# Performance work log

Measured on AMD Instinct MI355X. Metric: run time of the kernel, lower is better.

## Reference

```python
import jax, jax.numpy as jnp
import numpy as np

B, T, D = 2, 2048, 1024
H = 16
HD = D // H            # 64 head_dim
DL = 512               # d_latent
NR = 64                # n_rope
EPS = 1.1920929e-07    # torch.finfo(float32).eps (nn.RMSNorm default)


def _rms_norm(x, w):
    # x: (..., HD); RMSNorm: x / sqrt(mean(x^2)+eps) * w
    ms = jnp.mean(jnp.square(x), axis=-1, keepdims=True)
    return x * jax.lax.rsqrt(ms + EPS) * w


def setup_inputs() -> dict:
    key = jax.random.key(0)
    ks = jax.random.split(key, 10)
    s = 0.02
    return {
        "x": jax.random.normal(ks[0], (B, T, D), dtype=jnp.float32),
        "W_DQ": jax.random.normal(ks[1], (DL, HD), dtype=jnp.float32) * s,
        "W_UQ": jax.random.normal(ks[2], (HD, DL), dtype=jnp.float32) * s,
        "W_DKV": jax.random.normal(ks[3], (2 * DL, HD), dtype=jnp.float32) * s,
        "W_UKV": jax.random.normal(ks[4], (2 * HD, 2 * DL), dtype=jnp.float32) * s,
        "W_QR": jax.random.normal(ks[5], (NR, HD), dtype=jnp.float32) * s,
        "W_KR": jax.random.normal(ks[6], (NR, HD), dtype=jnp.float32) * s,
        "W_O": jax.random.normal(ks[7], (HD, HD), dtype=jnp.float32) * s,
        "q_norm_w": jnp.ones((HD,), dtype=jnp.float32),
        "k_norm_w": jnp.ones((HD,), dtype=jnp.float32),
    }


def reference(x, W_DQ, W_UQ, W_DKV, W_UKV, W_QR, W_KR, W_O, q_norm_w, k_norm_w):
    b, t, d = x.shape
    scale = HD ** (-0.5)
    # (B, H, T, HD)
    xh = x.reshape(b, t, H, HD).transpose(0, 2, 1, 3)
    # latent down/up projections (Linear: y = x @ W.T)
    c_q = jnp.einsum('bhtd,ld->bhtl', xh, W_DQ)              # (B,H,T,DL)
    q_c = jnp.einsum('bhtl,dl->bhtd', c_q, W_UQ)             # (B,H,T,HD)
    q_c_norm = _rms_norm(q_c, q_norm_w)
    q_r = jnp.einsum('bhtd,rd->bhtr', q_c_norm, W_QR)        # rope = identity
    q = jnp.concatenate([q_c_norm, q_r], axis=-1)            # (B,H,T,HD+NR)

    c_kv = jnp.einsum('bhtd,ld->bhtl', xh, W_DKV)            # (B,H,T,2DL)
    kv = jnp.einsum('bhtl,dl->bhtd', c_kv, W_UKV)            # (B,H,T,2HD)
    k_c, v_c = kv[..., :HD], kv[..., HD:]
    k_c_norm = _rms_norm(k_c, k_norm_w)
    k_r = jnp.einsum('bhtd,rd->bhtr', xh, W_KR)              # rope = identity
    k = jnp.concatenate([k_c_norm, k_r], axis=-1)            # (B,H,T,HD+NR)

    scores = jnp.einsum('bhqd,bhkd->bhqk', q, k) * scale     # (B,H,T,T)
    causal = jnp.triu(jnp.full((t, t), -jnp.inf, dtype=scores.dtype), k=1)
    attn = jax.nn.softmax(scores + causal, axis=-1)
    ctx = jnp.einsum('bhqk,bhkd->bhqd', attn, v_c)           # (B,H,T,HD)
    out = jnp.einsum('bhtd,od->bhto', ctx, W_O)
    return out.transpose(0, 2, 1, 3).reshape(b, t, d)
```

## Files before the change

kernel.cpp:

```cpp
#include <hip/hip_runtime.h>
#include <hip/hip_bf16.h>
#include <math.h>

namespace {

constexpr int T  = 2048;
constexpr int HD = 64;
constexpr float EPS = 1.1920929e-07f;
constexpr float PS = 0.125f * 1.44269504f;

constexpr int OFF_DQ  = 0;
constexpr int OFF_UQ  = 32768;
constexpr int OFF_DKV = 65536;
constexpr int OFF_UKV = 131072;
constexpr int OFF_QR  = 262144;
constexpr int OFF_KR  = 266240;
constexpr int OFF_O   = 270336;
constexpr int W_TOTAL = 274432;

typedef __attribute__((ext_vector_type(8))) short bf8v;
typedef __attribute__((ext_vector_type(4))) float f4v;

#define MFMA16(a, b, c) __builtin_amdgcn_mfma_f32_16x16x32_bf16((a), (b), (c), 0, 0, 0)

__device__ __forceinline__ short f2bf(float f) {
  union { float f; unsigned u; } v; v.f = f;
  unsigned r = v.u + 0x7FFFu + ((v.u >> 16) & 1u);
  return (short)(r >> 16);
}

__device__ __forceinline__ f4v z4() { f4v z = {0.f, 0.f, 0.f, 0.f}; return z; }

__device__ __forceinline__ int swz128(int b) { return b ^ (((b >> 7) & 7) << 4); }
__device__ __forceinline__ int swz256(int b) { return b ^ (((b >> 8) & 7) << 4); }

__device__ __forceinline__ bf8v ldA128(const short* lds, int row, int k) {
  return *(const bf8v*)((const char*)lds + swz128(row * 128 + k * 2));
}
__device__ __forceinline__ bf8v ldA256(const short* lds, int row, int k) {
  return *(const bf8v*)((const char*)lds + swz256(row * 256 + k * 2));
}

__device__ __forceinline__ void stage64x64(short* lds, const short* src, int stride, int tid) {
#pragma unroll
  for (int p = 0; p < 2; ++p) {
    int ci = tid + p * 256;
    int r = ci >> 3, c = (ci & 7) << 3;
    bf8v v = *(const bf8v*)(src + (size_t)r * stride + c);
    *(bf8v*)((char*)lds + swz128(ci * 16)) = v;
  }
}
__device__ __forceinline__ void stage128x64(short* lds, const short* src, int stride, int tid) {
#pragma unroll
  for (int p = 0; p < 4; ++p) {
    int ci = tid + p * 256;
    int r = ci >> 3, c = (ci & 7) << 3;
    bf8v v = *(const bf8v*)(src + (size_t)r * stride + c);
    *(bf8v*)((char*)lds + swz128(ci * 16)) = v;
  }
}

__device__ __forceinline__ void scat128(short* lds, int row0, int lane, int nt, f4v v) {
  int col = nt * 16 + (lane & 15);
  int r0 = row0 + ((lane >> 4) << 2);
#pragma unroll
  for (int r = 0; r < 4; ++r)
    *(short*)((char*)lds + swz128((r0 + r) * 128 + col * 2)) = f2bf(v[r]);
}
__device__ __forceinline__ void scat256(short* lds, int row0, int lane, int col, f4v v) {
  int r0 = row0 + ((lane >> 4) << 2);
#pragma unroll
  for (int r = 0; r < 4; ++r)
    *(short*)((char*)lds + swz256((r0 + r) * 256 + col * 2)) = f2bf(v[r]);
}

__device__ __forceinline__ void gload_lds16(const void* g, void* l) {
  __builtin_amdgcn_global_load_lds(
      (const __attribute__((address_space(1))) void*)g,
      (__attribute__((address_space(3))) void*)l, 16, 0, 0);
}

__global__ __launch_bounds__(256) void cvt_x_kernel(const float* __restrict__ x,
                                                    short* __restrict__ xb) {
  int i = (blockIdx.x * 256 + threadIdx.x) * 4;
  float4 v = *(const float4*)(x + i);
  int d = i & 1023, t = (i >> 10) & 2047, b = i >> 21;
  int h = d >> 6, dd = d & 63;
  short4 o;
  o.x = f2bf(v.x); o.y = f2bf(v.y); o.z = f2bf(v.z); o.w = f2bf(v.w);
  *(short4*)(xb + ((((size_t)b * 16 + h) * T + t) * 64 + dd)) = o;
}

__global__ __launch_bounds__(256) void cvt_w_kernel(
    const float* __restrict__ W_DQ, const float* __restrict__ W_UQ,
    const float* __restrict__ W_DKV, const float* __restrict__ W_UKV,
    const float* __restrict__ W_QR, const float* __restrict__ W_KR,
    const float* __restrict__ W_O, short* __restrict__ wb) {
  int i = blockIdx.x * 256 + threadIdx.x;
  const float* src; int off;
  if      (i < 32768)  { src = W_DQ;  off = 0; }
  else if (i < 65536)  { src = W_UQ;  off = 32768; }
  else if (i < 131072) { src = W_DKV; off = 65536; }
  else if (i < 262144) { src = W_UKV; off = 131072; }
  else if (i < 266240) { src = W_QR;  off = 262144; }
  else if (i < 270336) { src = W_KR;  off = 266240; }
  else                 { src = W_O;   off = 270336; }
  wb[i] = f2bf(src[i - off]);
}

__global__ __launch_bounds__(256) void proj_q_mfma(
    const short* __restrict__ xb, const short* __restrict__ wb,
    const float* __restrict__ qnw, short* __restrict__ qb) {
  __shared__ __attribute__((aligned(16))) short Xs[64 * 64];
  __shared__ __attribute__((aligned(16))) short Wd[64 * 64];
  __shared__ __attribute__((aligned(16))) short Wu[64 * 64];
  __shared__ __attribute__((aligned(16))) short Cs[64 * 64];
  __shared__ __attribute__((aligned(16))) short Qr[64 * 64];

  const int tid = threadIdx.x, lane = tid & 63, w = tid >> 6;
  const int bh = blockIdx.y, t0 = blockIdx.x * 64;
  const int arow = w * 16 + (lane & 15);
  const int koff = (lane >> 4) << 3;

  stage64x64(Xs, xb + ((size_t)bh * T + t0) * 64, 64, tid);

  f4v acc[4];
#pragma unroll
  for (int nt = 0; nt < 4; ++nt) acc[nt] = z4();

  for (int lc = 0; lc < 8; ++lc) {
    const int l0 = lc * 64;
    __syncthreads();
    stage64x64(Wd, wb + OFF_DQ + (size_t)l0 * 64, 64, tid);
    stage64x64(Wu, wb + OFF_UQ + l0, 512, tid);
    __syncthreads();
    f4v cc[4];
#pragma unroll
    for (int nt = 0; nt < 4; ++nt) cc[nt] = z4();
#pragma unroll
    for (int ks = 0; ks < 2; ++ks) {
      bf8v a = ldA128(Xs, arow, ks * 32 + koff);
#pragma unroll
      for (int nt = 0; nt < 4; ++nt) {
        bf8v b = ldA128(Wd, nt * 16 + (lane & 15), ks * 32 + koff);
        cc[nt] = MFMA16(a, b, cc[nt]);
      }
    }
#pragma unroll
    for (int nt = 0; nt < 4; ++nt) scat128(Cs, w * 16, lane, nt, cc[nt]);
#pragma unroll
    for (int ks = 0; ks < 2; ++ks) {
      bf8v a = ldA128(Cs, arow, ks * 32 + koff);
#pragma unroll
      for (int nt = 0; nt < 4; ++nt) {
        bf8v b = ldA128(Wu, nt * 16 + (lane & 15), ks * 32 + koff);
        acc[nt] = MFMA16(a, b, acc[nt]);
      }
    }
  }

  float w4[4];
#pragma unroll
  for (int nt = 0; nt < 4; ++nt) w4[nt] = qnw[nt * 16 + (lane & 15)] * PS;
  f4v qn[4];
#pragma unroll
  for (int r = 0; r < 4; ++r) {
    float ss = 0.f;
#pragma unroll
    for (int nt = 0; nt < 4; ++nt) ss += acc[nt][r] * acc[nt][r];
    ss += __shfl_xor(ss, 1, 16); ss += __shfl_xor(ss, 2, 16);
    ss += __shfl_xor(ss, 4, 16); ss += __shfl_xor(ss, 8, 16);
    float inv = rsqrtf(ss * (1.f / 64.f) + EPS);
#pragma unroll
    for (int nt = 0; nt < 4; ++nt) qn[nt][r] = acc[nt][r] * inv * w4[nt];
  }

  __syncthreads();
#pragma unroll
  for (int nt = 0; nt < 4; ++nt) scat128(Cs, w * 16, lane, nt, qn[nt]);
  stage64x64(Wd, wb + OFF_QR, 64, tid);
  __syncthreads();

  f4v qr[4];
#pragma unroll
  for (int nt = 0; nt < 4; ++nt) qr[nt] = z4();
#pragma unroll
  for (int ks = 0; ks < 2; ++ks) {
    bf8v a = ldA128(Cs, arow, ks * 32 + koff);
#pragma unroll
    for (int nt = 0; nt < 4; ++nt) {
      bf8v b = ldA128(Wd, nt * 16 + (lane & 15), ks * 32 + koff);
      qr[nt] = MFMA16(a, b, qr[nt]);
    }
  }
#pragma unroll
  for (int nt = 0; nt < 4; ++nt) scat128(Qr, w * 16, lane, nt, qr[nt]);
  __syncthreads();

  short* qdst = qb + ((size_t)bh * T + t0) * 128;
#pragma unroll
  for (int p = 0; p < 2; ++p) {
    int ci = tid + p * 256;
    int r = ci >> 3, c = (ci & 7) << 3;
    *(bf8v*)(qdst + (size_t)r * 128 + c) =
        *(const bf8v*)((const char*)Cs + swz128(ci * 16));
    *(bf8v*)(qdst + (size_t)r * 128 + 64 + c) =
        *(const bf8v*)((const char*)Qr + swz128(ci * 16));
  }
}

__global__ __launch_bounds__(256) void proj_kv_mfma(
    const short* __restrict__ xb, const short* __restrict__ wb,
    const float* __restrict__ knw, short* __restrict__ kb, short* __restrict__ vtg) {
  __shared__ __attribute__((aligned(16))) short Xs[64 * 64];
  __shared__ __attribute__((aligned(16))) short Wd[64 * 64];
  __shared__ __attribute__((aligned(16))) short Cs[64 * 64];
  __shared__ __attribute__((aligned(16))) short Wu[128 * 64];
  __shared__ __attribute__((aligned(16))) short Ko[64 * 128];
  __shared__ __attribute__((aligned(16))) short Vt[64 * 64];

  const int tid = threadIdx.x, lane = tid & 63, w = tid >> 6;
  const int bh = blockIdx.y, t0 = blockIdx.x * 64;
  const int arow = w * 16 + (lane & 15);
  const int koff = (lane >> 4) << 3;

  stage64x64(Xs, xb + ((size_t)bh * T + t0) * 64, 64, tid);

  f4v acc[8];
#pragma unroll
  for (int nt = 0; nt < 8; ++nt) acc[nt] = z4();

  for (int lc = 0; lc < 16; ++lc) {
    const int l0 = lc * 64;
    __syncthreads();
    stage64x64(Wd, wb + OFF_DKV + (size_t)l0 * 64, 64, tid);
    stage128x64(Wu, wb + OFF_UKV + l0, 1024, tid);
    __syncthreads();
    f4v cc[4];
#pragma unroll
    for (int nt = 0; nt < 4; ++nt) cc[nt] = z4();
#pragma unroll
    for (int ks = 0; ks < 2; ++ks) {
      bf8v a = ldA128(Xs, arow, ks * 32 + koff);
#pragma unroll
      for (int nt = 0; nt < 4; ++nt) {
        bf8v b = ldA128(Wd, nt * 16 + (lane & 15), ks * 32 + koff);
        cc[nt] = MFMA16(a, b, cc[nt]);
      }
    }
#pragma unroll
    for (int nt = 0; nt < 4; ++nt) scat128(Cs, w * 16, lane, nt, cc[nt]);
#pragma unroll
    for (int ks = 0; ks < 2; ++ks) {
      bf8v a = ldA128(Cs, arow, ks * 32 + koff);
#pragma unroll
      for (int nt = 0; nt < 8; ++nt) {
        bf8v b = ldA128(Wu, nt * 16 + (lane & 15), ks * 32 + koff);
        acc[nt] = MFMA16(a, b, acc[nt]);
      }
    }
  }

  float w4[4];
#pragma unroll
  for (int nt = 0; nt < 4; ++nt) w4[nt] = knw[nt * 16 + (lane & 15)];
#pragma unroll
  for (int r = 0; r < 4; ++r) {
    float ss = 0.f;
#pragma unroll
    for (int nt = 0; nt < 4; ++nt) ss += acc[nt][r] * acc[nt][r];
    ss += __shfl_xor(ss, 1, 16); ss += __shfl_xor(ss, 2, 16);
    ss += __shfl_xor(ss, 4, 16); ss += __shfl_xor(ss, 8, 16);
    float inv = rsqrtf(ss * (1.f / 64.f) + EPS);
#pragma unroll
    for (int nt = 0; nt < 4; ++nt) acc[nt][r] *= inv * w4[nt];
  }
#pragma unroll
  for (int nt = 0; nt < 4; ++nt) scat256(Ko, w * 16, lane, nt * 16 + (lane & 15), acc[nt]);
#pragma unroll
  for (int nt = 0; nt < 4; ++nt) {
    int d = nt * 16 + (lane & 15);
    int tl0 = w * 16 + ((lane >> 4) << 2);
#pragma unroll
    for (int r = 0; r < 4; ++r)
      *(short*)((char*)Vt + swz128(d * 128 + (tl0 + r) * 2)) = f2bf(acc[4 + nt][r]);
  }

  __syncthreads();
  stage64x64(Wd, wb + OFF_KR, 64, tid);
  __syncthreads();
  f4v kr[4];
#pragma unroll
  for (int nt = 0; nt < 4; ++nt) kr[nt] = z4();
#pragma unroll
  for (int ks = 0; ks < 2; ++ks) {
    bf8v a = ldA128(Xs, arow, ks * 32 + koff);
#pragma unroll
    for (int nt = 0; nt < 4; ++nt) {
      bf8v b = ldA128(Wd, nt * 16 + (lane & 15), ks * 32 + koff);
      kr[nt] = MFMA16(a, b, kr[nt]);
    }
  }
#pragma unroll
  for (int nt = 0; nt < 4; ++nt) scat256(Ko, w * 16, lane, 64 + nt * 16 + (lane & 15), kr[nt]);
  __syncthreads();

  short* kdst = kb + ((size_t)bh * T + t0) * 128;
#pragma unroll
  for (int p = 0; p < 4; ++p) {
    int ci = tid + p * 256;
    int r = ci >> 4, c = (ci & 15) << 3;
    *(bf8v*)(kdst + (size_t)r * 128 + c) =
        *(const bf8v*)((const char*)Ko + swz256(ci * 16));
  }
#pragma unroll
  for (int p = 0; p < 2; ++p) {
    int ci = tid + p * 256;
    int d = ci >> 3, c = (ci & 7) << 3;
    *(bf8v*)(vtg + ((size_t)bh * 64 + d) * T + t0 + c) =
        *(const bf8v*)((const char*)Vt + swz128(ci * 16));
  }
}

__global__ __launch_bounds__(256) void attn_mfma(
    const short* __restrict__ qb, const short* __restrict__ kb,
    const short* __restrict__ vtg, const short* __restrict__ wb,
    float* __restrict__ out) {
  __shared__ __attribute__((aligned(16))) short Ks[3][64 * 128];
  __shared__ __attribute__((aligned(16))) short Vs[2][64 * 64];
  __shared__ __attribute__((aligned(16))) short Ps[64 * 64];

  const int tid = threadIdx.x, lane = tid & 63, w = tid >> 6;
  const int lin = blockIdx.y * 16 + blockIdx.x;
  const int xcd = lin & 7, slot = lin >> 3;
  const int bh = xcd + 8 * (slot >> 4);
  const int px = slot & 15;
  const int qtA = px, qtB = 31 - px;
  const int cntA = qtA + 1;
  const int NT = 33;

  const int b = bh >> 4, h = bh & 15;
  const int c16 = lane & 15;
  const int g4 = lane >> 4;
  const int koff = g4 << 3;
  const int rg4 = g4 << 2;
  const int lbase = lane & 48;

  const short* kbh = kb + (size_t)bh * T * 128;
  const short* vbh = vtg + (size_t)bh * 64 * T;

  bf8v aqA[4], aqB[4], bwo[2][4];
  {
    const short* qA = qb + ((size_t)bh * T + qtA * 64 + w * 16 + c16) * 128;
    const short* qB = qb + ((size_t)bh * T + qtB * 64 + w * 16 + c16) * 128;
#pragma unroll
    for (int ks = 0; ks < 4; ++ks) {
      aqA[ks] = *(const bf8v*)(qA + ks * 32 + koff);
      aqB[ks] = *(const bf8v*)(qB + ks * 32 + koff);
    }
#pragma unroll
    for (int ks = 0; ks < 2; ++ks)
#pragma unroll
      for (int nt = 0; nt < 4; ++nt)
        bwo[ks][nt] = *(const bf8v*)(wb + OFF_O + (size_t)(nt * 16 + c16) * 64 +
                                     ks * 32 + koff);
  }

  auto ktile = [&](int gg) { return (gg < NT) ? ((gg < cntA) ? gg : gg - cntA) : 0; };

  auto stageK = [&](int gg) {
    const int jt = ktile(gg);
    const char* src = (const char*)(kbh + jt * 64 * 128);
    char* dst = (char*)&Ks[gg % 3][0];
#pragma unroll
    for (int p = 0; p < 4; ++p) {
      const int base = p * 256 + w * 64;
      gload_lds16(src + swz256((base + lane) * 16), dst + base * 16);
    }
  };
  auto stageV = [&](int gg) {
    const int jt = ktile(gg);
    char* dst = (char*)&Vs[gg & 1][0];
#pragma unroll
    for (int p = 0; p < 2; ++p) {
      const int base = p * 256 + w * 64;
      const int tb = swz128((base + lane) * 16);
      const int r = tb >> 7, cb = tb & 127;
      gload_lds16((const char*)vbh + ((size_t)r * T + jt * 64) * 2 + cb,
                  dst + base * 16);
    }
  };

  stageK(0);
  stageK(1);
  stageV(0);
  asm volatile("s_waitcnt vmcnt(6)" ::: "memory");
  __builtin_amdgcn_s_barrier();
  __builtin_amdgcn_sched_barrier(0);

  int gg = 0;
  float* obase = out + (size_t)b * T * 1024 + h * 64;

  auto run_seg = [&](const int qt, const bf8v(&aq)[4]) {
    const int t0 = qt * 64;
    const int lrow = w * 16 + rg4;
    const int qglob = t0 + w * 16 + c16;

    f4v ctx[4];
    float m = -INFINITY, l = 0.f;
#pragma unroll
    for (int nt = 0; nt < 4; ++nt) ctx[nt] = z4();

    for (int jt = 0; jt <= qt; ++jt, ++gg) {
      const short* Kb = &Ks[gg % 3][0];
      const short* Vb = &Vs[gg & 1][0];
      stageK(gg + 2);
      stageV(gg + 1);

      const int j0 = jt * 64;
      const bool diag = (jt == qt);

      f4v s[4];
#pragma unroll
      for (int nt = 0; nt < 4; ++nt) s[nt] = z4();
#pragma unroll
      for (int ks = 0; ks < 4; ++ks) {
#pragma unroll
        for (int nt = 0; nt < 4; ++nt) {
          bf8v bk = ldA256(Kb, nt * 16 + c16, ks * 32 + koff);
          s[nt] = MFMA16(bk, aq[ks], s[nt]);
        }
      }

      if (diag) {
#pragma unroll
        for (int nt = 0; nt < 4; ++nt)
#pragma unroll
          for (int r = 0; r < 4; ++r)
            if (j0 + nt * 16 + rg4 + r > qglob) s[nt][r] = -INFINITY;
      }

      f4v mnt;
#pragma unroll
      for (int r = 0; r < 4; ++r)
        mnt[r] = fmaxf(fmaxf(s[0][r], s[1][r]), fmaxf(s[2][r], s[3][r]));
      float mx = fmaxf(fmaxf(mnt[0], mnt[1]), fmaxf(mnt[2], mnt[3]));
      mx = fmaxf(mx, __shfl_xor(mx, 16));
      mx = fmaxf(mx, __shfl_xor(mx, 32));

      if (__any(mx - m > 8.f)) {
        const float mn  = fmaxf(m, mx);
        const float scl = __builtin_amdgcn_exp2f(m - mn);
        l *= scl; m = mn;
        float sr[4];
#pragma unroll
        for (int r = 0; r < 4; ++r) sr[r] = __shfl(scl, lbase + rg4 + r);
#pragma unroll
        for (int nt = 0; nt < 4; ++nt)
#pragma unroll
          for (int r = 0; r < 4; ++r) ctx[nt][r] *= sr[r];
      }

#pragma unroll
      for (int nt = 0; nt < 4; ++nt)
#pragma unroll
        for (int r = 0; r < 4; ++r)
          s[nt][r] = __builtin_amdgcn_exp2f(s[nt][r] - m);
      f4v sv = s[0] + s[1] + s[2] + s[3];
      float rs = (sv[0] + sv[1]) + (sv[2] + sv[3]);
      rs += __shfl_xor(rs, 16);
      rs += __shfl_xor(rs, 32);
      l += rs;

      {
        char* prow = (char*)Ps;
        const int rbase = (w * 16 + c16) * 128 + koff;
#pragma unroll
        for (int nt = 0; nt < 4; ++nt) {
          __hip_bfloat162 h0 = __float22bfloat162_rn(make_float2(s[nt][0], s[nt][1]));
          __hip_bfloat162 h1 = __float22bfloat162_rn(make_float2(s[nt][2], s[nt][3]));
          uint2 d;
          d.x = *(unsigned int*)&h0;
          d.y = *(unsigned int*)&h1;
          *(uint2*)(prow + swz128(rbase + nt * 32)) = d;
        }
      }

      asm volatile("s_waitcnt vmcnt(6)" ::: "memory");
      __builtin_amdgcn_sched_barrier(0);

#pragma unroll
      for (int ks = 0; ks < 2; ++ks) {
        bf8v pa = ldA128(Ps, w * 16 + c16, ks * 32 + koff);
#pragma unroll
        for (int nt = 0; nt < 4; ++nt) {
          bf8v vf = ldA128(Vb, nt * 16 + c16, ks * 32 + koff);
          ctx[nt] = MFMA16(pa, vf, ctx[nt]);
        }
      }

      __builtin_amdgcn_s_barrier();
      __builtin_amdgcn_sched_barrier(0);
    }

    float linv[4];
#pragma unroll
    for (int r = 0; r < 4; ++r) linv[r] = 1.0f / __shfl(l, lbase + rg4 + r);
    f4v cn[4];
#pragma unroll
    for (int nt = 0; nt < 4; ++nt)
#pragma unroll
      for (int r = 0; r < 4; ++r) cn[nt][r] = ctx[nt][r] * linv[r];
#pragma unroll
    for (int nt = 0; nt < 4; ++nt) scat128(Ps, w * 16, lane, nt, cn[nt]);

    f4v o[4];
#pragma unroll
    for (int nt = 0; nt < 4; ++nt) o[nt] = z4();
#pragma unroll
    for (int ks = 0; ks < 2; ++ks) {
      bf8v pa = ldA128(Ps, w * 16 + c16, ks * 32 + koff);
#pragma unroll
      for (int nt = 0; nt < 4; ++nt) o[nt] = MFMA16(pa, bwo[ks][nt], o[nt]);
    }

#pragma unroll
    for (int nt = 0; nt < 4; ++nt) {
#pragma unroll
      for (int r = 0; r < 4; ++r)
        obase[(size_t)(t0 + lrow + r) * 1024 + nt * 16 + c16] = o[nt][r];
    }
  };

  run_seg(qtA, aqA);
  run_seg(qtB, aqB);
}

}

extern "C" void kernel_launch(void* const* d_in, const int* in_sizes, int n_in,
                              void* d_out, int out_size, void* d_ws, size_t ws_size,
                              hipStream_t stream) {
  (void)in_sizes; (void)n_in; (void)out_size; (void)ws_size;
  const float* x     = (const float*)d_in[0];
  const float* W_DQ  = (const float*)d_in[1];
  const float* W_UQ  = (const float*)d_in[2];
  const float* W_DKV = (const float*)d_in[3];
  const float* W_UKV = (const float*)d_in[4];
  const float* W_QR  = (const float*)d_in[5];
  const float* W_KR  = (const float*)d_in[6];
  const float* W_O   = (const float*)d_in[7];
  const float* qnw   = (const float*)d_in[8];
  const float* knw   = (const float*)d_in[9];
  float* out = (float*)d_out;

  short* ws = (short*)d_ws;
  short* xb  = ws;
  short* qb  = ws + (size_t)4194304;
  short* kb  = ws + (size_t)12582912;
  short* vtg = ws + (size_t)20971520;
  short* wb  = ws + (size_t)25165824;

  cvt_x_kernel<<<4096, 256, 0, stream>>>(x, xb);
  cvt_w_kernel<<<W_TOTAL / 256, 256, 0, stream>>>(W_DQ, W_UQ, W_DKV, W_UKV,
                                                  W_QR, W_KR, W_O, wb);
  dim3 grid(T / 64, 32);
  proj_q_mfma<<<grid, 256, 0, stream>>>(xb, wb, qnw, qb);
  proj_kv_mfma<<<grid, 256, 0, stream>>>(xb, wb, knw, kb, vtg);
  dim3 agrid(16, 32);
  attn_mfma<<<agrid, 256, 0, stream>>>(qb, kb, vtg, wb, out);
}
```

Before: 149.7 us.

## Double-buffer projection weights via async LDS loads and widen projection tiles

Result: faster. 132.1 us (-11.7%).

```diff
diff --git a/kernel.cpp b/kernel.cpp
--- a/kernel.cpp
+++ b/kernel.cpp
@@ -23,6 +23,14 @@
 
 #define MFMA16(a, b, c) __builtin_amdgcn_mfma_f32_16x16x32_bf16((a), (b), (c), 0, 0, 0)
 
+#define HARD_BARRIER()                                   \
+  do {                                                   \
+    asm volatile("" ::: "memory");                       \
+    __builtin_amdgcn_s_barrier();                        \
+    asm volatile("" ::: "memory");                       \
+    __builtin_amdgcn_sched_barrier(0);                   \
+  } while (0)
+
 __device__ __forceinline__ short f2bf(float f) {
   union { float f; unsigned u; } v; v.f = f;
   unsigned r = v.u + 0x7FFFu + ((v.u >> 16) & 1u);
@@ -39,25 +47,6 @@
 }
 __device__ __forceinline__ bf8v ldA256(const short* lds, int row, int k) {
   return *(const bf8v*)((const char*)lds + swz256(row * 256 + k * 2));
-}
-
-__device__ __forceinline__ void stage64x64(short* lds, const short* src, int stride, int tid) {
-#pragma unroll
-  for (int p = 0; p < 2; ++p) {
-    int ci = tid + p * 256;
-    int r = ci >> 3, c = (ci & 7) << 3;
-    bf8v v = *(const bf8v*)(src + (size_t)r * stride + c);
-    *(bf8v*)((char*)lds + swz128(ci * 16)) = v;
-  }
-}
-__device__ __forceinline__ void stage128x64(short* lds, const short* src, int stride, int tid) {
-#pragma unroll
-  for (int p = 0; p < 4; ++p) {
-    int ci = tid + p * 256;
-    int r = ci >> 3, c = (ci & 7) << 3;
-    bf8v v = *(const bf8v*)(src + (size_t)r * stride + c);
-    *(bf8v*)((char*)lds + swz128(ci * 16)) = v;
-  }
 }
 
 __device__ __forceinline__ void scat128(short* lds, int row0, int lane, int nt, f4v v) {
@@ -111,214 +100,332 @@
 __global__ __launch_bounds__(256) void proj_q_mfma(
     const short* __restrict__ xb, const short* __restrict__ wb,
     const float* __restrict__ qnw, short* __restrict__ qb) {
-  __shared__ __attribute__((aligned(16))) short Xs[64 * 64];
-  __shared__ __attribute__((aligned(16))) short Wd[64 * 64];
-  __shared__ __attribute__((aligned(16))) short Wu[64 * 64];
-  __shared__ __attribute__((aligned(16))) short Cs[64 * 64];
-  __shared__ __attribute__((aligned(16))) short Qr[64 * 64];
+  __shared__ __attribute__((aligned(16))) short Xs[128 * 64];
+  __shared__ __attribute__((aligned(16))) short Wd[2][64 * 64];
+  __shared__ __attribute__((aligned(16))) short Wu[2][64 * 64];
+  __shared__ __attribute__((aligned(16))) short Cs[128 * 64];
 
   const int tid = threadIdx.x, lane = tid & 63, w = tid >> 6;
-  const int bh = blockIdx.y, t0 = blockIdx.x * 64;
-  const int arow = w * 16 + (lane & 15);
+  const int bh = blockIdx.y, t0 = blockIdx.x * 128;
+  const int c16 = lane & 15;
   const int koff = (lane >> 4) << 3;
 
-  stage64x64(Xs, xb + ((size_t)bh * T + t0) * 64, 64, tid);
-
-  f4v acc[4];
-#pragma unroll
-  for (int nt = 0; nt < 4; ++nt) acc[nt] = z4();
+  auto stageWd = [&](int lc) {
+    const char* src = (const char*)(wb + OFF_DQ + lc * 64 * 64);
+    char* dst = (char*)&Wd[lc & 1][0];
+#pragma unroll
+    for (int p = 0; p < 2; ++p) {
+      const int base = p * 256 + w * 64;
+      gload_lds16(src + swz128((base + lane) * 16), dst + base * 16);
+    }
+  };
+  auto stageWu = [&](int lc) {
+    const char* src = (const char*)(wb + OFF_UQ + lc * 64);
+    char* dst = (char*)&Wu[lc & 1][0];
+#pragma unroll
+    for (int p = 0; p < 2; ++p) {
+      const int base = p * 256 + w * 64;
+      const int lb = swz128((base + lane) * 16);
+      gload_lds16(src + (size_t)(lb >> 7) * 1024 + (lb & 127), dst + base * 16);
+    }
+  };
+
+  {
+    const char* src = (const char*)(xb + ((size_t)bh * T + t0) * 64);
+#pragma unroll
+    for (int p = 0; p < 4; ++p) {
+      const int base = p * 256 + w * 64;
+      gload_lds16(src + swz128((base + lane) * 16), (char*)Xs + base * 16);
+    }
+  }
+  stageWd(0);
+  stageWu(0);
+  __syncthreads();
+
+  f4v acc[2][4];
+#pragma unroll
+  for (int rg = 0; rg < 2; ++rg)
+#pragma unroll
+    for (int nt = 0; nt < 4; ++nt) acc[rg][nt] = z4();
 
   for (int lc = 0; lc < 8; ++lc) {
-    const int l0 = lc * 64;
+    if (lc < 7) { stageWd(lc + 1); stageWu(lc + 1); }
+    else {
+      const char* src = (const char*)(wb + OFF_QR);
+      char* dst = (char*)&Wd[0][0];
+#pragma unroll
+      for (int p = 0; p < 2; ++p) {
+        const int base = p * 256 + w * 64;
+        gload_lds16(src + swz128((base + lane) * 16), dst + base * 16);
+      }
+    }
+    const short* Wdc = &Wd[lc & 1][0];
+    const short* Wuc = &Wu[lc & 1][0];
+
+    f4v cc[2][4];
+#pragma unroll
+    for (int rg = 0; rg < 2; ++rg)
+#pragma unroll
+      for (int nt = 0; nt < 4; ++nt) cc[rg][nt] = z4();
+#pragma unroll
+    for (int rg = 0; rg < 2; ++rg)
+#pragma unroll
+      for (int ks = 0; ks < 2; ++ks) {
+        bf8v a = ldA128(Xs, w * 32 + rg * 16 + c16, ks * 32 + koff);
+#pragma unroll
+        for (int nt = 0; nt < 4; ++nt) {
+          bf8v b = ldA128(Wdc, nt * 16 + c16, ks * 32 + koff);
+          cc[rg][nt] = MFMA16(a, b, cc[rg][nt]);
+        }
+      }
+#pragma unroll
+    for (int rg = 0; rg < 2; ++rg)
+#pragma unroll
+      for (int nt = 0; nt < 4; ++nt) scat128(Cs, w * 32 + rg * 16, lane, nt, cc[rg][nt]);
+#pragma unroll
+    for (int rg = 0; rg < 2; ++rg)
+#pragma unroll
+      for (int ks = 0; ks < 2; ++ks) {
+        bf8v a = ldA128(Cs, w * 32 + rg * 16 + c16, ks * 32 + koff);
+#pragma unroll
+        for (int nt = 0; nt < 4; ++nt) {
+          bf8v b = ldA128(Wuc, nt * 16 + c16, ks * 32 + koff);
+          acc[rg][nt] = MFMA16(a, b, acc[rg][nt]);
+        }
+      }
     __syncthreads();
-    stage64x64(Wd, wb + OFF_DQ + (size_t)l0 * 64, 64, tid);
-    stage64x64(Wu, wb + OFF_UQ + l0, 512, tid);
-    __syncthreads();
-    f4v cc[4];
-#pragma unroll
-    for (int nt = 0; nt < 4; ++nt) cc[nt] = z4();
+  }
+
+  float w4[4];
+#pragma unroll
+  for (int nt = 0; nt < 4; ++nt) w4[nt] = qnw[nt * 16 + c16] * PS;
+#pragma unroll
+  for (int rg = 0; rg < 2; ++rg)
+#pragma unroll
+    for (int r = 0; r < 4; ++r) {
+      float ss = 0.f;
+#pragma unroll
+      for (int nt = 0; nt < 4; ++nt) ss += acc[rg][nt][r] * acc[rg][nt][r];
+      ss += __shfl_xor(ss, 1, 16); ss += __shfl_xor(ss, 2, 16);
+      ss += __shfl_xor(ss, 4, 16); ss += __shfl_xor(ss, 8, 16);
+      float inv = rsqrtf(ss * (1.f / 64.f) + EPS);
+#pragma unroll
+      for (int nt = 0; nt < 4; ++nt) acc[rg][nt][r] *= inv * w4[nt];
+    }
+
+#pragma unroll
+  for (int rg = 0; rg < 2; ++rg)
+#pragma unroll
+    for (int nt = 0; nt < 4; ++nt) scat128(Cs, w * 32 + rg * 16, lane, nt, acc[rg][nt]);
+
+  f4v qr[2][4];
+#pragma unroll
+  for (int rg = 0; rg < 2; ++rg)
+#pragma unroll
+    for (int nt = 0; nt < 4; ++nt) qr[rg][nt] = z4();
+#pragma unroll
+  for (int rg = 0; rg < 2; ++rg)
 #pragma unroll
     for (int ks = 0; ks < 2; ++ks) {
-      bf8v a = ldA128(Xs, arow, ks * 32 + koff);
+      bf8v a = ldA128(Cs, w * 32 + rg * 16 + c16, ks * 32 + koff);
 #pragma unroll
       for (int nt = 0; nt < 4; ++nt) {
-        bf8v b = ldA128(Wd, nt * 16 + (lane & 15), ks * 32 + koff);
-        cc[nt] = MFMA16(a, b, cc[nt]);
-      }
-    }
-#pragma unroll
-    for (int nt = 0; nt < 4; ++nt) scat128(Cs, w * 16, lane, nt, cc[nt]);
-#pragma unroll
-    for (int ks = 0; ks < 2; ++ks) {
-      bf8v a = ldA128(Cs, arow, ks * 32 + koff);
-#pragma unroll
-      for (int nt = 0; nt < 4; ++nt) {
-        bf8v b = ldA128(Wu, nt * 16 + (lane & 15), ks * 32 + koff);
-        acc[nt] = MFMA16(a, b, acc[nt]);
-      }
-    }
-  }
-
-  float w4[4];
-#pragma unroll
-  for (int nt = 0; nt < 4; ++nt) w4[nt] = qnw[nt * 16 + (lane & 15)] * PS;
-  f4v qn[4];
-#pragma unroll
-  for (int r = 0; r < 4; ++r) {
-    float ss = 0.f;
-#pragma unroll
-    for (int nt = 0; nt < 4; ++nt) ss += acc[nt][r] * acc[nt][r];
-    ss += __shfl_xor(ss, 1, 16); ss += __shfl_xor(ss, 2, 16);
-    ss += __shfl_xor(ss, 4, 16); ss += __shfl_xor(ss, 8, 16);
-    float inv = rsqrtf(ss * (1.f / 64.f) + EPS);
-#pragma unroll
-    for (int nt = 0; nt < 4; ++nt) qn[nt][r] = acc[nt][r] * inv * w4[nt];
-  }
-
+        bf8v b = ldA128(&Wd[0][0], nt * 16 + c16, ks * 32 + koff);
+        qr[rg][nt] = MFMA16(a, b, qr[rg][nt]);
+      }
+    }
+#pragma unroll
+  for (int rg = 0; rg < 2; ++rg)
+#pragma unroll
+    for (int nt = 0; nt < 4; ++nt) scat128(Xs, w * 32 + rg * 16, lane, nt, qr[rg][nt]);
   __syncthreads();
-#pragma unroll
-  for (int nt = 0; nt < 4; ++nt) scat128(Cs, w * 16, lane, nt, qn[nt]);
-  stage64x64(Wd, wb + OFF_QR, 64, tid);
-  __syncthreads();
-
-  f4v qr[4];
-#pragma unroll
-  for (int nt = 0; nt < 4; ++nt) qr[nt] = z4();
-#pragma unroll
-  for (int ks = 0; ks < 2; ++ks) {
-    bf8v a = ldA128(Cs, arow, ks * 32 + koff);
-#pragma unroll
-    for (int nt = 0; nt < 4; ++nt) {
-      bf8v b = ldA128(Wd, nt * 16 + (lane & 15), ks * 32 + koff);
-      qr[nt] = MFMA16(a, b, qr[nt]);
-    }
-  }
-#pragma unroll
-  for (int nt = 0; nt < 4; ++nt) scat128(Qr, w * 16, lane, nt, qr[nt]);
-  __syncthreads();
 
   short* qdst = qb + ((size_t)bh * T + t0) * 128;
 #pragma unroll
-  for (int p = 0; p < 2; ++p) {
+  for (int p = 0; p < 4; ++p) {
     int ci = tid + p * 256;
     int r = ci >> 3, c = (ci & 7) << 3;
     *(bf8v*)(qdst + (size_t)r * 128 + c) =
         *(const bf8v*)((const char*)Cs + swz128(ci * 16));
     *(bf8v*)(qdst + (size_t)r * 128 + 64 + c) =
-        *(const bf8v*)((const char*)Qr + swz128(ci * 16));
+        *(const bf8v*)((const char*)Xs + swz128(ci * 16));
   }
 }
 
 __global__ __launch_bounds__(256) void proj_kv_mfma(
     const short* __restrict__ xb, const short* __restrict__ wb,
     const float* __restrict__ knw, short* __restrict__ kb, short* __restrict__ vtg) {
-  __shared__ __attribute__((aligned(16))) short Xs[64 * 64];
-  __shared__ __attribute__((aligned(16))) short Wd[64 * 64];
-  __shared__ __attribute__((aligned(16))) short Cs[64 * 64];
-  __shared__ __attribute__((aligned(16))) short Wu[128 * 64];
-  __shared__ __attribute__((aligned(16))) short Ko[64 * 128];
-  __shared__ __attribute__((aligned(16))) short Vt[64 * 64];
+  __shared__ __attribute__((aligned(16))) short Xs[128 * 64];
+  __shared__ __attribute__((aligned(16))) short Wd[2][64 * 64];
+  __shared__ __attribute__((aligned(16))) short Wu[2][128 * 64];
+  __shared__ __attribute__((aligned(16))) short Cs[128 * 64];
 
   const int tid = threadIdx.x, lane = tid & 63, w = tid >> 6;
-  const int bh = blockIdx.y, t0 = blockIdx.x * 64;
-  const int arow = w * 16 + (lane & 15);
-  const int koff = (lane >> 4) << 3;
-
-  stage64x64(Xs, xb + ((size_t)bh * T + t0) * 64, 64, tid);
-
-  f4v acc[8];
-#pragma unroll
-  for (int nt = 0; nt < 8; ++nt) acc[nt] = z4();
+  const int bh = blockIdx.y, t0 = blockIdx.x * 128;
+  const int c16 = lane & 15;
+  const int g4 = lane >> 4;
+  const int koff = g4 << 3;
+  const int rg4 = g4 << 2;
+
+  auto stageWd = [&](int lc) {
+    const char* src = (const char*)(wb + OFF_DKV + lc * 64 * 64);
+    char* dst = (char*)&Wd[lc & 1][0];
+#pragma unroll
+    for (int p = 0; p < 2; ++p) {
+      const int base = p * 256 + w * 64;
+      gload_lds16(src + swz128((base + lane) * 16), dst + base * 16);
+    }
+  };
+  auto stageWu = [&](int lc) {
+    const char* src = (const char*)(wb + OFF_UKV + lc * 64);
+    char* dst = (char*)&Wu[lc & 1][0];
+#pragma unroll
+    for (int p = 0; p < 4; ++p) {
+      const int base = p * 256 + w * 64;
+      const int lb = swz128((base + lane) * 16);
+      gload_lds16(src + (size_t)(lb >> 7) * 2048 + (lb & 127), dst + base * 16);
+    }
+  };
+
+  {
+    const char* src = (const char*)(xb + ((size_t)bh * T + t0) * 64);
+#pragma unroll
+    for (int p = 0; p < 4; ++p) {
+      const int base = p * 256 + w * 64;
+      gload_lds16(src + swz128((base + lane) * 16), (char*)Xs + base * 16);
+    }
+  }
+  stageWd(0);
+  stageWu(0);
+  __syncthreads();
+
+  f4v acc[2][8];
+#pragma unroll
+  for (int rg = 0; rg < 2; ++rg)
+#pragma unroll
+    for (int nt = 0; nt < 8; ++nt) acc[rg][nt] = z4();
 
   for (int lc = 0; lc < 16; ++lc) {
-    const int l0 = lc * 64;
+    if (lc < 15) { stageWd(lc + 1); stageWu(lc + 1); }
+    else {
+      const char* src = (const char*)(wb + OFF_KR);
+      char* dst = (char*)&Wd[0][0];
+#pragma unroll
+      for (int p = 0; p < 2; ++p) {
+        const int base = p * 256 + w * 64;
+        gload_lds16(src + swz128((base + lane) * 16), dst + base * 16);
+      }
+    }
+    const short* Wdc = &Wd[lc & 1][0];
+    const short* Wuc = &Wu[lc & 1][0];
+
+    f4v cc[2][4];
+#pragma unroll
+    for (int rg = 0; rg < 2; ++rg)
+#pragma unroll
+      for (int nt = 0; nt < 4; ++nt) cc[rg][nt] = z4();
+#pragma unroll
+    for (int rg = 0; rg < 2; ++rg)
+#pragma unroll
+      for (int ks = 0; ks < 2; ++ks) {
+        bf8v a = ldA128(Xs, w * 32 + rg * 16 + c16, ks * 32 + koff);
+#pragma unroll
+        for (int nt = 0; nt < 4; ++nt) {
+          bf8v b = ldA128(Wdc, nt * 16 + c16, ks * 32 + koff);
+          cc[rg][nt] = MFMA16(a, b, cc[rg][nt]);
+        }
+      }
+#pragma unroll
+    for (int rg = 0; rg < 2; ++rg)
+#pragma unroll
+      for (int nt = 0; nt < 4; ++nt) scat128(Cs, w * 32 + rg * 16, lane, nt, cc[rg][nt]);
+#pragma unroll
+    for (int rg = 0; rg < 2; ++rg)
+#pragma unroll
+      for (int ks = 0; ks < 2; ++ks) {
+        bf8v a = ldA128(Cs, w * 32 + rg * 16 + c16, ks * 32 + koff);
+#pragma unroll
+        for (int nt = 0; nt < 8; ++nt) {
+          bf8v b = ldA128(Wuc, nt * 16 + c16, ks * 32 + koff);
+          acc[rg][nt] = MFMA16(a, b, acc[rg][nt]);
+        }
+      }
     __syncthreads();
-    stage64x64(Wd, wb + OFF_DKV + (size_t)l0 * 64, 64, tid);
-    stage128x64(Wu, wb + OFF_UKV + l0, 1024, tid);
-    __syncthreads();
-    f4v cc[4];
-#pragma unroll
-    for (int nt = 0; nt < 4; ++nt) cc[nt] = z4();
+  }
+
+  float w4[4];
+#pragma unroll
+  for (int nt = 0; nt < 4; ++nt) w4[nt] = knw[nt * 16 + c16];
+#pragma unroll
+  for (int rg = 0; rg < 2; ++rg)
+#pragma unroll
+    for (int r = 0; r < 4; ++r) {
+      float ss = 0.f;
+#pragma unroll
+      for (int nt = 0; nt < 4; ++nt) ss += acc[rg][nt][r] * acc[rg][nt][r];
+      ss += __shfl_xor(ss, 1, 16); ss += __shfl_xor(ss, 2, 16);
+      ss += __shfl_xor(ss, 4, 16); ss += __shfl_xor(ss, 8, 16);
+      float inv = rsqrtf(ss * (1.f / 64.f) + EPS);
+#pragma unroll
+      for (int nt = 0; nt < 4; ++nt) acc[rg][nt][r] *= inv * w4[nt];
+    }
+
+  short* Ko = &Wu[0][0];
+#pragma unroll
+  for (int rg = 0; rg < 2; ++rg)
+#pragma unroll
+    for (int nt = 0; nt < 4; ++nt)
+      scat256(Ko, w * 32 + rg * 16, lane, nt * 16 + c16, acc[rg][nt]);
+
+#pragma unroll
+  for (int rg = 0; rg < 2; ++rg)
+#pragma unroll
+    for (int nt = 0; nt < 4; ++nt) {
+      const int d = nt * 16 + c16;
+      const int tc0 = w * 32 + rg * 16 + rg4;
+#pragma unroll
+      for (int r = 0; r < 4; ++r)
+        *(short*)((char*)Cs + swz256(d * 256 + (tc0 + r) * 2)) =
+            f2bf(acc[rg][4 + nt][r]);
+    }
+
+  f4v kr[2][4];
+#pragma unroll
+  for (int rg = 0; rg < 2; ++rg)
+#pragma unroll
+    for (int nt = 0; nt < 4; ++nt) kr[rg][nt] = z4();
+#pragma unroll
+  for (int rg = 0; rg < 2; ++rg)
 #pragma unroll
     for (int ks = 0; ks < 2; ++ks) {
-      bf8v a = ldA128(Xs, arow, ks * 32 + koff);
+      bf8v a = ldA128(Xs, w * 32 + rg * 16 + c16, ks * 32 + koff);
 #pragma unroll
       for (int nt = 0; nt < 4; ++nt) {
-        bf8v b = ldA128(Wd, nt * 16 + (lane & 15), ks * 32 + koff);
-        cc[nt] = MFMA16(a, b, cc[nt]);
-      }
-    }
-#pragma unroll
-    for (int nt = 0; nt < 4; ++nt) scat128(Cs, w * 16, lane, nt, cc[nt]);
-#pragma unroll
-    for (int ks = 0; ks < 2; ++ks) {
-      bf8v a = ldA128(Cs, arow, ks * 32 + koff);
-#pragma unroll
-      for (int nt = 0; nt < 8; ++nt) {
-        bf8v b = ldA128(Wu, nt * 16 + (lane & 15), ks * 32 + koff);
-        acc[nt] = MFMA16(a, b, acc[nt]);
-      }
-    }
-  }
-
-  float w4[4];
-#pragma unroll
-  for (int nt = 0; nt < 4; ++nt) w4[nt] = knw[nt * 16 + (lane & 15)];
-#pragma unroll
-  for (int r = 0; r < 4; ++r) {
-    float ss = 0.f;
-#pragma unroll
-    for (int nt = 0; nt < 4; ++nt) ss += acc[nt][r] * acc[nt][r];
-    ss += __shfl_xor(ss, 1, 16); ss += __shfl_xor(ss, 2, 16);
-    ss += __shfl_xor(ss, 4, 16); ss += __shfl_xor(ss, 8, 16);
-    float inv = rsqrtf(ss * (1.f / 64.f) + EPS);
-#pragma unroll
-    for (int nt = 0; nt < 4; ++nt) acc[nt][r] *= inv * w4[nt];
-  }
-#pragma unroll
-  for (int nt = 0; nt < 4; ++nt) scat256(Ko, w * 16, lane, nt * 16 + (lane & 15), acc[nt]);
-#pragma unroll
-  for (int nt = 0; nt < 4; ++nt) {
-    int d = nt * 16 + (lane & 15);
-    int tl0 = w * 16 + ((lane >> 4) << 2);
-#pragma unroll
-    for (int r = 0; r < 4; ++r)
-      *(short*)((char*)Vt + swz128(d * 128 + (tl0 + r) * 2)) = f2bf(acc[4 + nt][r]);
-  }
-
+        bf8v b = ldA128(&Wd[0][0], nt * 16 + c16, ks * 32 + koff);
+        kr[rg][nt] = MFMA16(a, b, kr[rg][nt]);
+      }
+    }
+#pragma unroll
+  for (int rg = 0; rg < 2; ++rg)
+#pragma unroll
+    for (int nt = 0; nt < 4; ++nt)
+      scat256(Ko, w * 32 + rg * 16, lane, 64 + nt * 16 + c16, kr[rg][nt]);
   __syncthreads();
-  stage64x64(Wd, wb + OFF_KR, 64, tid);
-  __syncthreads();
-  f4v kr[4];
-#pragma unroll
-  for (int nt = 0; nt < 4; ++nt) kr[nt] = z4();
-#pragma unroll
-  for (int ks = 0; ks < 2; ++ks) {
-    bf8v a = ldA128(Xs, arow, ks * 32 + koff);
-#pragma unroll
-    for (int nt = 0; nt < 4; ++nt) {
-      bf8v b = ldA128(Wd, nt * 16 + (lane & 15), ks * 32 + koff);
-      kr[nt] = MFMA16(a, b, kr[nt]);
-    }
-  }
-#pragma unroll
-  for (int nt = 0; nt < 4; ++nt) scat256(Ko, w * 16, lane, 64 + nt * 16 + (lane & 15), kr[nt]);
-  __syncthreads();
 
   short* kdst = kb + ((size_t)bh * T + t0) * 128;
 #pragma unroll
-  for (int p = 0; p < 4; ++p) {
+  for (int p = 0; p < 8; ++p) {
     int ci = tid + p * 256;
     int r = ci >> 4, c = (ci & 15) << 3;
     *(bf8v*)(kdst + (size_t)r * 128 + c) =
         *(const bf8v*)((const char*)Ko + swz256(ci * 16));
   }
 #pragma unroll
-  for (int p = 0; p < 2; ++p) {
+  for (int p = 0; p < 4; ++p) {
     int ci = tid + p * 256;
-    int d = ci >> 3, c = (ci & 7) << 3;
+    int d = ci >> 4, c = (ci & 15) << 3;
     *(bf8v*)(vtg + ((size_t)bh * 64 + d) * T + t0 + c) =
-        *(const bf8v*)((const char*)Vt + swz128(ci * 16));
+        *(const bf8v*)((const char*)Cs + swz256(ci * 16));
   }
 }
 
@@ -395,8 +502,7 @@
   stageK(1);
   stageV(0);
   asm volatile("s_waitcnt vmcnt(6)" ::: "memory");
-  __builtin_amdgcn_s_barrier();
-  __builtin_amdgcn_sched_barrier(0);
+  HARD_BARRIER();
 
   int gg = 0;
   float* obase = out + (size_t)b * T * 1024 + h * 64;
@@ -487,7 +593,7 @@
       }
 
       asm volatile("s_waitcnt vmcnt(6)" ::: "memory");
-      __builtin_amdgcn_sched_barrier(0);
+      HARD_BARRIER();
 
 #pragma unroll
       for (int ks = 0; ks < 2; ++ks) {
@@ -499,8 +605,7 @@
         }
       }
 
-      __builtin_amdgcn_s_barrier();
-      __builtin_amdgcn_sched_barrier(0);
+      HARD_BARRIER();
     }
 
     float linv[4];
@@ -564,9 +669,9 @@
   cvt_x_kernel<<<4096, 256, 0, stream>>>(x, xb);
   cvt_w_kernel<<<W_TOTAL / 256, 256, 0, stream>>>(W_DQ, W_UQ, W_DKV, W_UKV,
                                                   W_QR, W_KR, W_O, wb);
-  dim3 grid(T / 64, 32);
-  proj_q_mfma<<<grid, 256, 0, stream>>>(xb, wb, qnw, qb);
-  proj_kv_mfma<<<grid, 256, 0, stream>>>(xb, wb, knw, kb, vtg);
+  dim3 pgrid(T / 128, 32);
+  proj_q_mfma<<<pgrid, 256, 0, stream>>>(xb, wb, qnw, qb);
+  proj_kv_mfma<<<pgrid, 256, 0, stream>>>(xb, wb, knw, kb, vtg);
   dim3 agrid(16, 32);
   attn_mfma<<<agrid, 256, 0, stream>>>(qb, kb, vtg, wb, out);
 }
```
